# Kernel tuning notes

Measured on AMD Instinct MI355X. Metric: run time of the kernel, lower is better.

Reference implementation:

```python
import jax, jax.numpy as jnp
import numpy as np

EPS = 1e-5
K = 20
MAXV = 64


def knn_idx(x, k):
    # x: [B,N,D] -> idx: [B,N,k] (excluding self, matching torch topk of -dist)
    xx = jnp.sum(x * x, axis=-1, keepdims=True)                      # [B,N,1]
    dist = xx - 2.0 * jnp.einsum('bnd,bmd->bnm', x, x) + jnp.swapaxes(xx, 1, 2)
    _, idx = jax.lax.top_k(-dist, k + 1)
    return idx[:, :, 1:]


def edge_conv(x, W, gamma, beta, mean, var, k):
    # x: [B,N,C]; W: [O,2C]; BN in eval mode; max over k neighbors
    idx = knn_idx(x, k)                                              # [B,N,k]
    nbr = jax.vmap(lambda xi, ii: xi[ii])(x, idx)                    # [B,N,k,C]
    ctr = jnp.broadcast_to(x[:, :, None, :], nbr.shape)
    ef = jnp.concatenate([ctr, nbr - ctr], axis=-1)                  # [B,N,k,2C]
    y = jnp.einsum('bnkc,oc->bnko', ef, W)                           # 1x1 conv
    y = (y - mean) * (gamma * jax.lax.rsqrt(var + EPS)) + beta       # BN eval
    y = jnp.where(y >= 0, y, 0.2 * y)                                # LeakyReLU
    return jnp.max(y, axis=2)                                        # [B,N,O]


def setup_inputs() -> dict:
    key = jax.random.key(0)
    ks = jax.random.split(key, 32)
    f32 = jnp.float32
    def w(k_, o, i):
        return jax.random.normal(k_, (o, i), f32) / np.float32(np.sqrt(i))
    def vec(k_, c):
        return jax.random.normal(k_, (c,), f32) * 0.1
    d = {}
    d['x'] = jax.random.normal(ks[0], (4, 8192, 5), f32)
    # EdgeConv 1: 5 -> 32
    d['W1'] = w(ks[1], 32, 10)
    d['g1'] = jax.random.uniform(ks[2], (32,), f32, 0.5, 1.5)
    d['b1'] = vec(ks[3], 32); d['m1'] = vec(ks[4], 32)
    d['v1'] = jax.random.uniform(ks[5], (32,), f32, 0.5, 1.5)
    # EdgeConv 2: 32 -> 64
    d['W2'] = w(ks[6], 64, 64)
    d['g2'] = jax.random.uniform(ks[7], (64,), f32, 0.5, 1.5)
    d['b2'] = vec(ks[8], 64); d['m2'] = vec(ks[9], 64)
    d['v2'] = jax.random.uniform(ks[10], (64,), f32, 0.5, 1.5)
    # EdgeConv 3: 64 -> 128
    d['W3'] = w(ks[11], 128, 128)
    d['g3'] = jax.random.uniform(ks[12], (128,), f32, 0.5, 1.5)
    d['b3'] = vec(ks[13], 128); d['m3'] = vec(ks[14], 128)
    d['v3'] = jax.random.uniform(ks[15], (128,), f32, 0.5, 1.5)
    # conv_global: 224 -> 256
    d['Wg'] = w(ks[16], 256, 224)
    d['gg'] = jax.random.uniform(ks[17], (256,), f32, 0.5, 1.5)
    d['bg'] = vec(ks[18], 256); d['mg'] = vec(ks[19], 256)
    d['vg'] = jax.random.uniform(ks[20], (256,), f32, 0.5, 1.5)
    # vertex predictor heads
    d['Wv1'] = w(ks[21], 512, 256); d['bv1'] = vec(ks[22], 512)
    d['Wv2'] = w(ks[23], 192, 512); d['bv2'] = vec(ks[24], 192)
    d['Wq1'] = w(ks[25], 64, 256); d['bq1'] = vec(ks[26], 64)
    d['Wq2'] = w(ks[27], 1, 64); d['bq2'] = vec(ks[28], 1)
    return d


def reference(x, W1, g1, b1, m1, v1, W2, g2, b2, m2, v2, W3, g3, b3, m3, v3,
              Wg, gg, bg, mg, vg, Wv1, bv1, Wv2, bv2, Wq1, bq1, Wq2, bq2):
    B = x.shape[0]
    x1 = edge_conv(x, W1, g1, b1, m1, v1, K)      # [B,N,32]
    x2 = edge_conv(x1, W2, g2, b2, m2, v2, K)     # [B,N,64]
    x3 = edge_conv(x2, W3, g3, b3, m3, v3, K)     # [B,N,128]
    x_concat = jnp.concatenate([x1, x2, x3], axis=2)               # [B,N,224]
    xg = jnp.einsum('bnc,oc->bno', x_concat, Wg)                   # 1x1 conv1d
    xg = (xg - mg) * (gg * jax.lax.rsqrt(vg + EPS)) + bg
    xg = jnp.where(xg >= 0, xg, 0.2 * xg)
    gfeat = jnp.max(xg, axis=1)                                    # [B,256]
    h = jax.nn.relu(gfeat @ Wv1.T + bv1)                           # Dropout=eval id
    vertex_coords = (h @ Wv2.T + bv2).reshape(B, MAXV, 3)
    q = jax.nn.relu(gfeat @ Wq1.T + bq1)
    nvs = jax.nn.sigmoid(q @ Wq2.T + bq2)                          # [B,1]
    num_vertices = jnp.clip(jnp.round(nvs * MAXV), 1, MAXV).astype(jnp.int32)
    return (vertex_coords, num_vertices[:, 0], nvs[:, 0], gfeat, x_concat)
```

## Files before the change

### kernel.cpp

```cpp
#include <hip/hip_runtime.h>
#include <hip/hip_bf16.h>


#define NPTS 8192
#define BATCH 4
#define KNBR 20

template <int D, int RS, int S, int TJ, int B>
__global__ __launch_bounds__(128) void knn_part(
    const float* feat, float* xcat) {
    __shared__ float xj[TJ * D];
    __shared__ float xxj[TJ];
    __shared__ float bufd[B * 128];
    __shared__ unsigned short bufj[B * 128];
    const int JC = NPTS / S;

    int gi = blockIdx.x * 128 + threadIdx.x;
    int s  = blockIdx.y;
    int b  = gi >> 13;
    int ib = gi & (NPTS - 1);
    const float* fb = feat + (size_t)b * NPTS * RS;
    int tid = threadIdx.x;

    float xi[D];
    if (D % 4 == 0) {
        #pragma unroll
        for (int c4 = 0; c4 < D / 4; ++c4) {
            float4 v = *(const float4*)(fb + (size_t)ib * RS + 4 * c4);
            xi[4 * c4] = v.x; xi[4 * c4 + 1] = v.y;
            xi[4 * c4 + 2] = v.z; xi[4 * c4 + 3] = v.w;
        }
    } else {
        #pragma unroll
        for (int c = 0; c < D; ++c) xi[c] = fb[(size_t)ib * RS + c];
    }
    float xxi = 0.f;
    #pragma unroll
    for (int c = 0; c < D; ++c) xxi = fmaf(xi[c], xi[c], xxi);

    float dl[21];
    int   il[21];
    #pragma unroll
    for (int t = 0; t < 21; ++t) { dl[t] = __builtin_inff(); il[t] = 0; }

    float thr = __builtin_inff();
    int   cnt = 0;

    for (int j0 = s * JC; j0 < (s + 1) * JC; j0 += TJ) {
        __syncthreads();
        if (D % 4 == 0) {
            for (int e = tid; e < TJ * (D / 4); e += 128) {
                int r = e / (D / 4), c4 = e % (D / 4);
                float4 v = *(const float4*)(fb + (size_t)(j0 + r) * RS + 4 * c4);
                *(float4*)(xj + r * D + 4 * c4) = v;
            }
        } else {
            for (int e = tid; e < TJ * D; e += 128) {
                int r = e / D, c = e % D;
                xj[e] = fb[(size_t)(j0 + r) * RS + c];
            }
        }
        if (tid < TJ) {
            const float* row = fb + (size_t)(j0 + tid) * RS;
            float sm = 0.f;
            if (D % 4 == 0) {
                #pragma unroll
                for (int c4 = 0; c4 < D / 4; ++c4) {
                    float4 v = *(const float4*)(row + 4 * c4);
                    sm = fmaf(v.x, v.x, sm); sm = fmaf(v.y, v.y, sm);
                    sm = fmaf(v.z, v.z, sm); sm = fmaf(v.w, v.w, sm);
                }
            } else {
                #pragma unroll
                for (int c = 0; c < D; ++c) sm = fmaf(row[c], row[c], sm);
            }
            xxj[tid] = sm;
        }
        __syncthreads();
        for (int jj = 0; jj < TJ; ++jj) {
            float dot = 0.f;
            if (D % 4 == 0) {
                const float* xr = xj + jj * D;
                #pragma unroll
                for (int c4 = 0; c4 < D / 4; ++c4) {
                    float4 v = *(const float4*)(xr + 4 * c4);
                    dot = fmaf(xi[4 * c4 + 0], v.x, dot);
                    dot = fmaf(xi[4 * c4 + 1], v.y, dot);
                    dot = fmaf(xi[4 * c4 + 2], v.z, dot);
                    dot = fmaf(xi[4 * c4 + 3], v.w, dot);
                }
            } else {
                #pragma unroll
                for (int c = 0; c < D; ++c) dot = fmaf(xi[c], xj[jj * D + c], dot);
            }
            float d = __builtin_fmaf(-2.f, dot, xxi + xxj[jj]);
            if (__any(cnt == B)) {
                for (int u = 0; u < B; ++u) {
                    if (u < cnt) {
                        float dd = bufd[u * 128 + tid];
                        int   jj2 = (int)bufj[u * 128 + tid];
                        if (dd < dl[20]) {
                            dl[20] = dd; il[20] = jj2;
                            #pragma unroll
                            for (int t = 20; t > 0; --t) {
                                if (dl[t] < dl[t - 1]) {
                                    float td = dl[t]; dl[t] = dl[t - 1]; dl[t - 1] = td;
                                    int   ti = il[t]; il[t] = il[t - 1]; il[t - 1] = ti;
                                }
                            }
                        }
                    }
                }
                cnt = 0;
                thr = dl[20];
            }
            if (d < thr) {
                bufd[cnt * 128 + tid] = d;
                bufj[cnt * 128 + tid] = (unsigned short)(j0 + jj);
                ++cnt;
            }
        }
    }
    for (int u = 0; u < B; ++u) {
        if (u < cnt) {
            float dd = bufd[u * 128 + tid];
            int   jj2 = (int)bufj[u * 128 + tid];
            if (dd < dl[20]) {
                dl[20] = dd; il[20] = jj2;
                #pragma unroll
                for (int t = 20; t > 0; --t) {
                    if (dl[t] < dl[t - 1]) {
                        float td = dl[t]; dl[t] = dl[t - 1]; dl[t - 1] = td;
                        int   ti = il[t]; il[t] = il[t - 1]; il[t - 1] = ti;
                    }
                }
            }
        }
    }
    unsigned short* cp =
        (unsigned short*)(xcat + (size_t)gi * 224 + 96) + s * 21;
    #pragma unroll
    for (int t = 0; t < 21; ++t) cp[t] = (unsigned short)il[t];
}

template <int D, int RS, int S>
__global__ __launch_bounds__(256) void knn_merge(
    const float* feat, const float* xcat, unsigned short* __restrict__ idxout) {
    int gi = blockIdx.x * 256 + threadIdx.x;
    int b  = gi >> 13;
    int ib = gi & (NPTS - 1);
    const float* fb = feat + (size_t)b * NPTS * RS;

    float xi[D];
    if (D % 4 == 0) {
        #pragma unroll
        for (int c4 = 0; c4 < D / 4; ++c4) {
            float4 v = *(const float4*)(fb + (size_t)ib * RS + 4 * c4);
            xi[4 * c4] = v.x; xi[4 * c4 + 1] = v.y;
            xi[4 * c4 + 2] = v.z; xi[4 * c4 + 3] = v.w;
        }
    } else {
        #pragma unroll
        for (int c = 0; c < D; ++c) xi[c] = fb[(size_t)ib * RS + c];
    }
    float xxi = 0.f;
    #pragma unroll
    for (int c = 0; c < D; ++c) xxi = fmaf(xi[c], xi[c], xxi);

    const unsigned short* cp =
        (const unsigned short*)(xcat + (size_t)gi * 224 + 96);

    float dl[21];
    int   il[21];
    #pragma unroll
    for (int t = 0; t < 21; ++t) { dl[t] = __builtin_inff(); il[t] = 0; }

    for (int t = 0; t < S * 21; ++t) {
        int j = ((int)cp[t]) & (NPTS - 1);
        const float* row = fb + (size_t)j * RS;
        float dot = 0.f, xx = 0.f;
        if (D % 4 == 0) {
            #pragma unroll
            for (int c4 = 0; c4 < D / 4; ++c4) {
                float4 v = *(const float4*)(row + 4 * c4);
                dot = fmaf(xi[4 * c4], v.x, dot);     xx = fmaf(v.x, v.x, xx);
                dot = fmaf(xi[4 * c4 + 1], v.y, dot); xx = fmaf(v.y, v.y, xx);
                dot = fmaf(xi[4 * c4 + 2], v.z, dot); xx = fmaf(v.z, v.z, xx);
                dot = fmaf(xi[4 * c4 + 3], v.w, dot); xx = fmaf(v.w, v.w, xx);
            }
        } else {
            #pragma unroll
            for (int c = 0; c < D; ++c) {
                float v = row[c];
                dot = fmaf(xi[c], v, dot);
                xx  = fmaf(v, v, xx);
            }
        }
        float d = __builtin_fmaf(-2.f, dot, xxi + xx);
        if (d < dl[20]) {
            dl[20] = d; il[20] = j;
            #pragma unroll
            for (int u = 20; u > 0; --u) {
                if (dl[u] < dl[u - 1]) {
                    float td = dl[u]; dl[u] = dl[u - 1]; dl[u - 1] = td;
                    int   ti = il[u]; il[u] = il[u - 1]; il[u - 1] = ti;
                }
            }
        }
    }
    unsigned short* op = idxout + (size_t)gi * KNBR;
    #pragma unroll
    for (int t = 1; t < 21; ++t) op[t - 1] = (unsigned short)il[t];
}

template <int CIN, int RS, int COUT, int OTILE, int P>
__global__ __launch_bounds__(256) void edgeconv_kernel(
    const float* feat, const unsigned short* __restrict__ knn,
    const float* __restrict__ W, const float* __restrict__ g,
    const float* __restrict__ beta, const float* __restrict__ mu,
    const float* __restrict__ var,
    float* outb, int concat_off) {
    __shared__ float diff[P][KNBR][CIN];
    __shared__ float xil[P][CIN];
    __shared__ unsigned short kidx[P * KNBR];
    __shared__ float sl[OTILE], bl[OTILE], ml[OTILE];

    int tid = threadIdx.x;
    int h   = blockIdx.y;
    int n0  = blockIdx.x * P;
    int b   = n0 >> 13;
    const float* fbase = feat + ((size_t)b << 13) * RS;

    for (int e = tid; e < P * CIN; e += 256)
        xil[e / CIN][e % CIN] = feat[(size_t)(n0 + e / CIN) * RS + e % CIN];
    for (int e = tid; e < P * KNBR; e += 256)
        kidx[e] = knn[(size_t)(n0 + e / KNBR) * KNBR + e % KNBR] & (NPTS - 1);
    for (int e = tid; e < OTILE; e += 256) {
        int o = h * OTILE + e;
        sl[e] = g[o] * rsqrtf(var[o] + 1e-5f);
        bl[e] = beta[o];
        ml[e] = mu[o];
    }
    __syncthreads();

    if (CIN % 4 == 0) {
        for (int e = tid; e < P * KNBR * (CIN / 4); e += 256) {
            int r = e / (CIN / 4), c4 = e % (CIN / 4);
            int p = r / KNBR, k = r % KNBR;
            int j = (int)kidx[r];
            float4 v = *(const float4*)(fbase + (size_t)j * RS + 4 * c4);
            diff[p][k][4 * c4 + 0] = v.x - xil[p][4 * c4 + 0];
            diff[p][k][4 * c4 + 1] = v.y - xil[p][4 * c4 + 1];
            diff[p][k][4 * c4 + 2] = v.z - xil[p][4 * c4 + 2];
            diff[p][k][4 * c4 + 3] = v.w - xil[p][4 * c4 + 3];
        }
    } else {
        for (int e = tid; e < P * KNBR * CIN; e += 256) {
            int r = e / CIN, c = e % CIN;
            int pp = r / KNBR, k = r % KNBR;
            int j = (int)kidx[r];
            diff[pp][k][c] = fbase[(size_t)j * RS + c] - xil[pp][c];
        }
    }
    __syncthreads();

    int ol = tid % OTILE, p = tid / OTILE;
    int o  = h * OTILE + ol;

    float wreg[CIN];
    #pragma unroll
    for (int c = 0; c < CIN; ++c) wreg[c] = W[(size_t)o * (2 * CIN) + c];
    float a = 0.f;
    #pragma unroll
    for (int c = 0; c < CIN; ++c) a = fmaf(wreg[c], xil[p][c], a);
    #pragma unroll
    for (int c = 0; c < CIN; ++c) wreg[c] = W[(size_t)o * (2 * CIN) + CIN + c];

    float s = sl[ol], mm = ml[ol], bb = bl[ol];
    float best = -__builtin_inff();
    for (int k = 0; k < KNBR; ++k) {
        float ac0 = a, ac1 = 0.f, ac2 = 0.f, ac3 = 0.f;
        #pragma unroll
        for (int c = 0; c < CIN; ++c) {
            float d = diff[p][k][c];
            if ((c & 3) == 0)      ac0 = fmaf(wreg[c], d, ac0);
            else if ((c & 3) == 1) ac1 = fmaf(wreg[c], d, ac1);
            else if ((c & 3) == 2) ac2 = fmaf(wreg[c], d, ac2);
            else                   ac3 = fmaf(wreg[c], d, ac3);
        }
        float acc = ((ac0 + ac1) + ac2) + ac3;
        float y = (acc - mm) * s + bb;
        y = (y >= 0.f) ? y : 0.2f * y;
        best = fmaxf(best, y);
    }
    outb[(size_t)(n0 + p) * 224 + concat_off + o] = best;
}

__global__ __launch_bounds__(256) void convglobal_kernel(
    const float* __restrict__ xcat,
    const float* __restrict__ Wg, const float* __restrict__ gg,
    const float* __restrict__ bg, const float* __restrict__ mg,
    const float* __restrict__ vg,
    float* __restrict__ partial) {
    const int KC = 56, PT = 64, OT = 64, ST = 68;
    __shared__ float flT[KC * ST];
    __shared__ float WlT[KC * ST];
    __shared__ float red[64 * 17];

    int tid = threadIdx.x;
    int oi  = tid & 15, pi = tid >> 4;
    int o0  = blockIdx.y * OT;
    int n0  = blockIdx.x * PT;
    int b   = n0 >> 13;
    int pchunk = blockIdx.x & 127;

    float acc[4][4];
    #pragma unroll
    for (int u = 0; u < 4; ++u)
        #pragma unroll
        for (int v = 0; v < 4; ++v) acc[u][v] = 0.f;

    for (int kc = 0; kc < 224; kc += KC) {
        __syncthreads();
        for (int e = tid; e < PT * (KC / 4); e += 256) {
            int p = e / (KC / 4), c4 = e % (KC / 4);
            float4 v = *(const float4*)(xcat + (size_t)(n0 + p) * 224 + kc + 4 * c4);
            flT[(4 * c4 + 0) * ST + p] = v.x;
            flT[(4 * c4 + 1) * ST + p] = v.y;
            flT[(4 * c4 + 2) * ST + p] = v.z;
            flT[(4 * c4 + 3) * ST + p] = v.w;
        }
        for (int e = tid; e < OT * (KC / 4); e += 256) {
            int o = e / (KC / 4), c4 = e % (KC / 4);
            float4 v = *(const float4*)(Wg + (size_t)(o0 + o) * 224 + kc + 4 * c4);
            WlT[(4 * c4 + 0) * ST + o] = v.x;
            WlT[(4 * c4 + 1) * ST + o] = v.y;
            WlT[(4 * c4 + 2) * ST + o] = v.z;
            WlT[(4 * c4 + 3) * ST + o] = v.w;
        }
        __syncthreads();
        #pragma unroll 8
        for (int c = 0; c < KC; ++c) {
            float4 w4 = *(const float4*)(WlT + c * ST + oi * 4);
            float4 f4 = *(const float4*)(flT + c * ST + pi * 4);
            acc[0][0] = fmaf(w4.x, f4.x, acc[0][0]);
            acc[0][1] = fmaf(w4.x, f4.y, acc[0][1]);
            acc[0][2] = fmaf(w4.x, f4.z, acc[0][2]);
            acc[0][3] = fmaf(w4.x, f4.w, acc[0][3]);
            acc[1][0] = fmaf(w4.y, f4.x, acc[1][0]);
            acc[1][1] = fmaf(w4.y, f4.y, acc[1][1]);
            acc[1][2] = fmaf(w4.y, f4.z, acc[1][2]);
            acc[1][3] = fmaf(w4.y, f4.w, acc[1][3]);
            acc[2][0] = fmaf(w4.z, f4.x, acc[2][0]);
            acc[2][1] = fmaf(w4.z, f4.y, acc[2][1]);
            acc[2][2] = fmaf(w4.z, f4.z, acc[2][2]);
            acc[2][3] = fmaf(w4.z, f4.w, acc[2][3]);
            acc[3][0] = fmaf(w4.w, f4.x, acc[3][0]);
            acc[3][1] = fmaf(w4.w, f4.y, acc[3][1]);
            acc[3][2] = fmaf(w4.w, f4.z, acc[3][2]);
            acc[3][3] = fmaf(w4.w, f4.w, acc[3][3]);
        }
    }
    #pragma unroll
    for (int u = 0; u < 4; ++u) {
        int oL = oi * 4 + u, o = o0 + oL;
        float s = gg[o] * rsqrtf(vg[o] + 1e-5f);
        float mm = mg[o], bb = bg[o];
        float best = -__builtin_inff();
        #pragma unroll
        for (int v = 0; v < 4; ++v) {
            float y = (acc[u][v] - mm) * s + bb;
            y = (y >= 0.f) ? y : 0.2f * y;
            best = fmaxf(best, y);
        }
        red[oL * 17 + pi] = best;
    }
    __syncthreads();
    if (tid < 64) {
        float best = -__builtin_inff();
        #pragma unroll
        for (int q = 0; q < 16; ++q) best = fmaxf(best, red[tid * 17 + q]);
        partial[((size_t)(b * 128 + pchunk)) * 256 + o0 + tid] = best;
    }
}

__global__ void reduce_gfeat_kernel(const float* __restrict__ partial,
                                    float* __restrict__ gfeat,
                                    float* __restrict__ outg) {
    int b = blockIdx.x, o = threadIdx.x;
    float best = -__builtin_inff();
    for (int ch = 0; ch < 128; ++ch)
        best = fmaxf(best, partial[((size_t)b * 128 + ch) * 256 + o]);
    gfeat[b * 256 + o] = best;
    outg[b * 256 + o]  = best;
}

__global__ __launch_bounds__(256) void heads_kernel(
    const float* __restrict__ gfeat,
    const float* __restrict__ Wv1, const float* __restrict__ bv1,
    const float* __restrict__ Wv2, const float* __restrict__ bv2,
    const float* __restrict__ Wq1, const float* __restrict__ bq1,
    const float* __restrict__ Wq2, const float* __restrict__ bq2,
    float* __restrict__ out) {
    int b = blockIdx.x, t = threadIdx.x;
    __shared__ float gf[256], h[512], q[64];
    gf[t] = gfeat[b * 256 + t];
    __syncthreads();
    for (int r = t; r < 512; r += 256) {
        float acc = bv1[r];
        for (int c = 0; c < 256; ++c) acc = fmaf(Wv1[r * 256 + c], gf[c], acc);
        h[r] = fmaxf(acc, 0.f);
    }
    __syncthreads();
    if (t < 192) {
        float acc = bv2[t];
        for (int c = 0; c < 512; ++c) acc = fmaf(Wv2[t * 512 + c], h[c], acc);
        out[b * 192 + t] = acc;
    } else {
        int r = t - 192;
        if (r < 64) {
            float acc = bq1[r];
            for (int c = 0; c < 256; ++c) acc = fmaf(Wq1[r * 256 + c], gf[c], acc);
            q[r] = fmaxf(acc, 0.f);
        }
    }
    __syncthreads();
    if (t == 0) {
        float acc = bq2[0];
        for (int c = 0; c < 64; ++c) acc = fmaf(Wq2[c], q[c], acc);
        float nv = 1.0f / (1.0f + expf(-acc));
        out[772 + b] = nv;
        float num = fminf(fmaxf(rintf(nv * 64.0f), 1.0f), 64.0f);
        out[768 + b] = num;
    }
}

extern "C" void kernel_launch(void* const* d_in, const int* in_sizes, int n_in,
                              void* d_out, int out_size, void* d_ws, size_t ws_size,
                              hipStream_t stream) {
    (void)in_sizes; (void)n_in; (void)out_size; (void)ws_size;
    const float* x   = (const float*)d_in[0];
    const float* W1  = (const float*)d_in[1];
    const float* g1  = (const float*)d_in[2];
    const float* b1  = (const float*)d_in[3];
    const float* m1  = (const float*)d_in[4];
    const float* v1  = (const float*)d_in[5];
    const float* W2  = (const float*)d_in[6];
    const float* g2  = (const float*)d_in[7];
    const float* b2  = (const float*)d_in[8];
    const float* m2  = (const float*)d_in[9];
    const float* v2  = (const float*)d_in[10];
    const float* W3  = (const float*)d_in[11];
    const float* g3  = (const float*)d_in[12];
    const float* b3  = (const float*)d_in[13];
    const float* m3  = (const float*)d_in[14];
    const float* v3  = (const float*)d_in[15];
    const float* Wg  = (const float*)d_in[16];
    const float* gg  = (const float*)d_in[17];
    const float* bg  = (const float*)d_in[18];
    const float* mg  = (const float*)d_in[19];
    const float* vg  = (const float*)d_in[20];
    const float* Wv1 = (const float*)d_in[21];
    const float* bv1 = (const float*)d_in[22];
    const float* Wv2 = (const float*)d_in[23];
    const float* bv2 = (const float*)d_in[24];
    const float* Wq1 = (const float*)d_in[25];
    const float* bq1 = (const float*)d_in[26];
    const float* Wq2 = (const float*)d_in[27];
    const float* bq2 = (const float*)d_in[28];

    float* out  = (float*)d_out;
    float* xcat = out + 1800;
    char* ws = (char*)d_ws;
    const int ROWS = BATCH * NPTS;

    unsigned short* idx  = (unsigned short*)(ws);
    float*          part = (float*)(ws);
    float*          gft  = (float*)(ws + 524288);

    knn_part<5, 5, 8, 128, 8><<<dim3(ROWS / 128, 8), 128, 0, stream>>>(x, xcat);
    knn_merge<5, 5, 8><<<ROWS / 256, 256, 0, stream>>>(x, xcat, idx);
    edgeconv_kernel<5, 5, 32, 32, 8>
        <<<dim3(ROWS / 8, 1), 256, 0, stream>>>(x, idx, W1, g1, b1, m1, v1, xcat, 0);

    knn_part<32, 224, 8, 128, 8><<<dim3(ROWS / 128, 8), 128, 0, stream>>>(xcat, xcat);
    knn_merge<32, 224, 8><<<ROWS / 256, 256, 0, stream>>>(xcat, xcat, idx);
    edgeconv_kernel<32, 224, 64, 64, 4>
        <<<dim3(ROWS / 4, 1), 256, 0, stream>>>(xcat, idx, W2, g2, b2, m2, v2, xcat, 32);

    knn_part<64, 224, 8, 64, 8><<<dim3(ROWS / 128, 8), 128, 0, stream>>>(xcat + 32, xcat);
    knn_merge<64, 224, 8><<<ROWS / 256, 256, 0, stream>>>(xcat + 32, xcat, idx);
    edgeconv_kernel<64, 224, 128, 64, 4>
        <<<dim3(ROWS / 4, 2), 256, 0, stream>>>(xcat + 32, idx, W3, g3, b3, m3, v3, xcat, 96);

    convglobal_kernel<<<dim3(ROWS / 64, 4), 256, 0, stream>>>(
        xcat, Wg, gg, bg, mg, vg, part);
    reduce_gfeat_kernel<<<BATCH, 256, 0, stream>>>(part, gft, out + 776);

    heads_kernel<<<BATCH, 256, 0, stream>>>(
        gft, Wv1, bv1, Wv2, bv2, Wq1, bq1, Wq2, bq2, out);
}
```

Before: 3.783 ms.

## Compute kNN candidate distances with bf16 MFMA and refine exactly in fp32

Replaces the scalar fp32 pairwise-distance loop in the partial kNN kernel with bf16 MFMA 16x16x32 tiles. The resulting distances are stored in swizzled shared memory and filtered against a threshold widened by a safety margin. Surviving candidates are buffered and recomputed exactly in fp32 before insertion into the per-thread top-21 list, so the ranking still comes from full-precision distances. This cuts VALU work for the distance computation, at the cost of larger shared-memory use, lower occupancy, and a margin-based filter that could drop true neighbours if bf16 error exceeds the bound.

```diff
diff --git a/kernel.cpp b/kernel.cpp
--- a/kernel.cpp
+++ b/kernel.cpp
@@ -6,21 +6,54 @@
 #define BATCH 4
 #define KNBR 20
 
-template <int D, int RS, int S, int TJ, int B>
-__global__ __launch_bounds__(128) void knn_part(
+typedef short bf16x8 __attribute__((ext_vector_type(8)));
+typedef float f32x4 __attribute__((ext_vector_type(4)));
+
+__device__ __forceinline__ unsigned short f2bf(float f) {
+    union { float f; unsigned u; } v; v.f = f;
+    unsigned r = v.u + 0x7fffu + ((v.u >> 16) & 1u);
+    return (unsigned short)(r >> 16);
+}
+
+__device__ __forceinline__ int cswz(int r, int nc) {
+    return (nc == 8) ? (r & 7) : ((r >> 1) & 3);
+}
+__device__ __forceinline__ int dswz(int q) { return (q >> 1) & 7; }
+
+template <int D, int DK, int RS, int S>
+__global__ __launch_bounds__(128) void knn_part_mfma(
     const float* feat, float* xcat) {
-    __shared__ float xj[TJ * D];
-    __shared__ float xxj[TJ];
-    __shared__ float bufd[B * 128];
-    __shared__ unsigned short bufj[B * 128];
-    const int JC = NPTS / S;
-
-    int gi = blockIdx.x * 128 + threadIdx.x;
-    int s  = blockIdx.y;
-    int b  = gi >> 13;
-    int ib = gi & (NPTS - 1);
+    constexpr int TJ  = 32;
+    constexpr int BUF = 16;
+    constexpr int JC  = NPTS / S;
+    constexpr int NC  = DK / 8;
+    constexpr int KS  = DK / 32;
+    constexpr int DSTR = 36;
+    constexpr int RSF = (D % 4 == 0) ? D : 9;
+    constexpr int REGA   = 18432;
+    constexpr int OFF_XJF = REGA;
+    constexpr int OFF_XJH = OFF_XJF + ((TJ * RSF * 4 + 15) & ~15);
+    constexpr int OFF_XXJ = OFF_XJH + TJ * DK * 2;
+    constexpr int OFF_BUF = OFF_XXJ + JC * 4;
+    constexpr int OFF_RED = OFF_BUF + BUF * 128 * 2;
+    __shared__ __align__(16) char smem[OFF_RED + 512];
+
+    float*          dist = (float*)smem;
+    unsigned short* xih  = (unsigned short*)smem;
+    float*          xjf  = (float*)(smem + OFF_XJF);
+    unsigned short* xjh  = (unsigned short*)(smem + OFF_XJH);
+    float*          xxj  = (float*)(smem + OFF_XXJ);
+    unsigned short* bufj = (unsigned short*)(smem + OFF_BUF);
+    float*          red  = (float*)(smem + OFF_RED);
+
+    const int tid   = threadIdx.x;
+    const int gi    = blockIdx.x * 128 + tid;
+    const int s     = blockIdx.y;
+    const int b     = gi >> 13;
+    const int ib    = gi & (NPTS - 1);
+    const int n0b   = (blockIdx.x * 128) & (NPTS - 1);
+    const int sbase = s * JC;
     const float* fb = feat + (size_t)b * NPTS * RS;
-    int tid = threadIdx.x;
 
     float xi[D];
     if (D % 4 == 0) {
@@ -38,105 +71,198 @@
     #pragma unroll
     for (int c = 0; c < D; ++c) xxi = fmaf(xi[c], xi[c], xxi);
 
+    for (int e = tid; e < 128 * NC; e += 128) {
+        int r = e / NC, c = e % NC;
+        const float* row = fb + (size_t)(n0b + r) * RS;
+        bf16x8 h;
+        if (D % 8 == 0) {
+            float4 v0 = *(const float4*)(row + c * 8);
+            float4 v1 = *(const float4*)(row + c * 8 + 4);
+            h[0] = (short)f2bf(v0.x); h[1] = (short)f2bf(v0.y);
+            h[2] = (short)f2bf(v0.z); h[3] = (short)f2bf(v0.w);
+            h[4] = (short)f2bf(v1.x); h[5] = (short)f2bf(v1.y);
+            h[6] = (short)f2bf(v1.z); h[7] = (short)f2bf(v1.w);
+        } else {
+            #pragma unroll
+            for (int t = 0; t < 8; ++t) {
+                int dim = c * 8 + t;
+                h[t] = (dim < D) ? (short)f2bf(row[dim]) : (short)0;
+            }
+        }
+        *(bf16x8*)(xih + (size_t)r * DK + (c ^ cswz(r, NC)) * 8) = h;
+    }
+
+    float mymax = 0.f;
+    for (int r = tid; r < JC; r += 128) {
+        const float* row = fb + (size_t)(sbase + r) * RS;
+        float sm = 0.f;
+        if (D % 4 == 0) {
+            #pragma unroll
+            for (int c4 = 0; c4 < D / 4; ++c4) {
+                float4 v = *(const float4*)(row + 4 * c4);
+                sm = fmaf(v.x, v.x, sm); sm = fmaf(v.y, v.y, sm);
+                sm = fmaf(v.z, v.z, sm); sm = fmaf(v.w, v.w, sm);
+            }
+        } else {
+            #pragma unroll
+            for (int c = 0; c < D; ++c) sm = fmaf(row[c], row[c], sm);
+        }
+        xxj[r] = sm;
+        mymax = fmaxf(mymax, sm);
+    }
+    red[tid] = mymax;
+    __syncthreads();
+
+    const int lane = tid & 63, wid = tid >> 6;
+    const int ln = lane & 15, lg = lane >> 4;
+    bf16x8 bfr[4][KS];
+    #pragma unroll
+    for (int qs = 0; qs < 4; ++qs)
+        #pragma unroll
+        for (int ks = 0; ks < KS; ++ks) {
+            int q = wid * 64 + qs * 16 + ln;
+            bfr[qs][ks] = *(const bf16x8*)(
+                xih + (size_t)q * DK + (((lg + 4 * ks) ^ cswz(q, NC)) * 8));
+        }
+
+    #pragma unroll
+    for (int off = 64; off >= 1; off >>= 1) {
+        if (tid < off) red[tid] = fmaxf(red[tid], red[tid + off]);
+        __syncthreads();
+    }
+    const float margin = 0.015625f * (xxi + red[0]);
+
     float dl[21];
     int   il[21];
     #pragma unroll
     for (int t = 0; t < 21; ++t) { dl[t] = __builtin_inff(); il[t] = 0; }
-
-    float thr = __builtin_inff();
+    float thr_s = __builtin_inff();
     int   cnt = 0;
-
-    for (int j0 = s * JC; j0 < (s + 1) * JC; j0 += TJ) {
-        __syncthreads();
-        if (D % 4 == 0) {
-            for (int e = tid; e < TJ * (D / 4); e += 128) {
-                int r = e / (D / 4), c4 = e % (D / 4);
-                float4 v = *(const float4*)(fb + (size_t)(j0 + r) * RS + 4 * c4);
-                *(float4*)(xj + r * D + 4 * c4) = v;
-            }
-        } else {
-            for (int e = tid; e < TJ * D; e += 128) {
-                int r = e / D, c = e % D;
-                xj[e] = fb[(size_t)(j0 + r) * RS + c];
-            }
-        }
-        if (tid < TJ) {
-            const float* row = fb + (size_t)(j0 + tid) * RS;
-            float sm = 0.f;
-            if (D % 4 == 0) {
-                #pragma unroll
-                for (int c4 = 0; c4 < D / 4; ++c4) {
-                    float4 v = *(const float4*)(row + 4 * c4);
-                    sm = fmaf(v.x, v.x, sm); sm = fmaf(v.y, v.y, sm);
-                    sm = fmaf(v.z, v.z, sm); sm = fmaf(v.w, v.w, sm);
+    int   j0s = 0;
+
+    auto drain = [&]() {
+        #pragma unroll 1
+        for (int u = 0; __any(u < cnt); ++u) {
+            if (u < cnt) {
+                int jsp = (int)bufj[u * 128 + tid];
+                int jl  = jsp - j0s;
+                const float* row = xjf + (size_t)jl * RSF;
+                float dot = 0.f;
+                if (D % 4 == 0) {
+                    int fsw = jl & 7;
+                    #pragma unroll
+                    for (int c4 = 0; c4 < D / 4; ++c4) {
+                        float4 v = *(const float4*)(row + ((c4 ^ fsw) * 4));
+                        dot = fmaf(xi[4 * c4 + 0], v.x, dot);
+                        dot = fmaf(xi[4 * c4 + 1], v.y, dot);
+                        dot = fmaf(xi[4 * c4 + 2], v.z, dot);
+                        dot = fmaf(xi[4 * c4 + 3], v.w, dot);
+                    }
+                } else {
+                    #pragma unroll
+                    for (int c = 0; c < D; ++c) dot = fmaf(xi[c], row[c], dot);
                 }
-            } else {
-                #pragma unroll
-                for (int c = 0; c < D; ++c) sm = fmaf(row[c], row[c], sm);
-            }
-            xxj[tid] = sm;
-        }
-        __syncthreads();
-        for (int jj = 0; jj < TJ; ++jj) {
-            float dot = 0.f;
-            if (D % 4 == 0) {
-                const float* xr = xj + jj * D;
-                #pragma unroll
-                for (int c4 = 0; c4 < D / 4; ++c4) {
-                    float4 v = *(const float4*)(xr + 4 * c4);
-                    dot = fmaf(xi[4 * c4 + 0], v.x, dot);
-                    dot = fmaf(xi[4 * c4 + 1], v.y, dot);
-                    dot = fmaf(xi[4 * c4 + 2], v.z, dot);
-                    dot = fmaf(xi[4 * c4 + 3], v.w, dot);
-                }
-            } else {
-                #pragma unroll
-                for (int c = 0; c < D; ++c) dot = fmaf(xi[c], xj[jj * D + c], dot);
-            }
-            float d = __builtin_fmaf(-2.f, dot, xxi + xxj[jj]);
-            if (__any(cnt == B)) {
-                for (int u = 0; u < B; ++u) {
-                    if (u < cnt) {
-                        float dd = bufd[u * 128 + tid];
-                        int   jj2 = (int)bufj[u * 128 + tid];
-                        if (dd < dl[20]) {
-                            dl[20] = dd; il[20] = jj2;
-                            #pragma unroll
-                            for (int t = 20; t > 0; --t) {
-                                if (dl[t] < dl[t - 1]) {
-                                    float td = dl[t]; dl[t] = dl[t - 1]; dl[t - 1] = td;
-                                    int   ti = il[t]; il[t] = il[t - 1]; il[t - 1] = ti;
-                                }
-                            }
+                float dd = __builtin_fmaf(-2.f, dot, xxi + xxj[jsp]);
+                if (dd < dl[20]) {
+                    dl[20] = dd; il[20] = sbase + jsp;
+                    #pragma unroll
+                    for (int t = 20; t > 0; --t) {
+                        if (dl[t] < dl[t - 1]) {
+                            float td = dl[t]; dl[t] = dl[t - 1]; dl[t - 1] = td;
+                            int   ti = il[t]; il[t] = il[t - 1]; il[t - 1] = ti;
                         }
                     }
                 }
-                cnt = 0;
-                thr = dl[20];
-            }
-            if (d < thr) {
-                bufd[cnt * 128 + tid] = d;
-                bufj[cnt * 128 + tid] = (unsigned short)(j0 + jj);
-                ++cnt;
-            }
-        }
-    }
-    for (int u = 0; u < B; ++u) {
-        if (u < cnt) {
-            float dd = bufd[u * 128 + tid];
-            int   jj2 = (int)bufj[u * 128 + tid];
-            if (dd < dl[20]) {
-                dl[20] = dd; il[20] = jj2;
+            }
+        }
+        cnt = 0;
+        thr_s = (dl[20] + margin) - xxi;
+    };
+
+    #pragma unroll 1
+    for (int t0 = 0; t0 < JC; t0 += TJ) {
+        j0s = t0;
+        __syncthreads();
+        if (D % 8 == 0) {
+            for (int e = tid; e < TJ * NC; e += 128) {
+                int r = e / NC, c = e % NC;
+                const float* row = fb + (size_t)(sbase + t0 + r) * RS + c * 8;
+                float4 v0 = *(const float4*)(row);
+                float4 v1 = *(const float4*)(row + 4);
+                int fsw = r & 7;
+                *(float4*)(xjf + (size_t)r * RSF + (((2 * c)     ^ fsw) * 4)) = v0;
+                *(float4*)(xjf + (size_t)r * RSF + (((2 * c + 1) ^ fsw) * 4)) = v1;
+                bf16x8 h;
+                h[0] = (short)f2bf(v0.x); h[1] = (short)f2bf(v0.y);
+                h[2] = (short)f2bf(v0.z); h[3] = (short)f2bf(v0.w);
+                h[4] = (short)f2bf(v1.x); h[5] = (short)f2bf(v1.y);
+                h[6] = (short)f2bf(v1.z); h[7] = (short)f2bf(v1.w);
+                *(bf16x8*)(xjh + (size_t)r * DK + ((c ^ cswz(r, NC)) * 8)) = h;
+            }
+        } else {
+            for (int e = tid; e < TJ * NC; e += 128) {
+                int r = e / NC, c = e % NC;
+                const float* row = fb + (size_t)(sbase + t0 + r) * RS;
+                bf16x8 h;
                 #pragma unroll
-                for (int t = 20; t > 0; --t) {
-                    if (dl[t] < dl[t - 1]) {
-                        float td = dl[t]; dl[t] = dl[t - 1]; dl[t - 1] = td;
-                        int   ti = il[t]; il[t] = il[t - 1]; il[t - 1] = ti;
-                    }
+                for (int q2 = 0; q2 < 8; ++q2) {
+                    int dim = c * 8 + q2;
+                    float f = (dim < D) ? row[dim] : 0.f;
+                    h[q2] = (short)f2bf(f);
+                    if (c == 0 && q2 < D) xjf[(size_t)r * RSF + q2] = f;
                 }
-            }
-        }
-    }
+                *(bf16x8*)(xjh + (size_t)r * DK + ((c ^ cswz(r, NC)) * 8)) = h;
+            }
+        }
+        __syncthreads();
+
+        #pragma unroll
+        for (int js = 0; js < TJ / 16; ++js) {
+            bf16x8 afr[KS];
+            #pragma unroll
+            for (int ks = 0; ks < KS; ++ks) {
+                int jr = js * 16 + ln;
+                afr[ks] = *(const bf16x8*)(
+                    xjh + (size_t)jr * DK +
+                    (((lg + 4 * ks) ^ cswz(jr, NC)) * 8));
+            }
+            float4 xj4 = *(const float4*)(xxj + t0 + js * 16 + lg * 4);
+            #pragma unroll
+            for (int qs = 0; qs < 4; ++qs) {
+                f32x4 acc = {0.f, 0.f, 0.f, 0.f};
+                #pragma unroll
+                for (int ks = 0; ks < KS; ++ks)
+                    acc = __builtin_amdgcn_mfma_f32_16x16x32_bf16(
+                        afr[ks], bfr[qs][ks], acc, 0, 0, 0);
+                float4 sv;
+                sv.x = __builtin_fmaf(-2.f, acc[0], xj4.x);
+                sv.y = __builtin_fmaf(-2.f, acc[1], xj4.y);
+                sv.z = __builtin_fmaf(-2.f, acc[2], xj4.z);
+                sv.w = __builtin_fmaf(-2.f, acc[3], xj4.w);
+                int q  = wid * 64 + qs * 16 + ln;
+                int ck = js * 4 + lg;
+                *(float4*)(dist + (size_t)q * DSTR + ((ck ^ dswz(q)) * 4)) = sv;
+            }
+        }
+        __syncthreads();
+
+        {
+            float* drow = dist + (size_t)tid * DSTR;
+            int dsw = dswz(tid);
+            #pragma unroll 1
+            for (int c = 0; c < TJ / 4; ++c) {
+                if (__any(cnt > BUF - 4)) drain();
+                float4 sv = *(const float4*)(drow + ((c ^ dsw) * 4));
+                int jb = t0 + c * 4;
+                if (sv.x < thr_s) { bufj[cnt * 128 + tid] = (unsigned short)(jb);     ++cnt; }
+                if (sv.y < thr_s) { bufj[cnt * 128 + tid] = (unsigned short)(jb + 1); ++cnt; }
+                if (sv.z < thr_s) { bufj[cnt * 128 + tid] = (unsigned short)(jb + 2); ++cnt; }
+                if (sv.w < thr_s) { bufj[cnt * 128 + tid] = (unsigned short)(jb + 3); ++cnt; }
+            }
+            drain();
+        }
+    }
+
     unsigned short* cp =
         (unsigned short*)(xcat + (size_t)gi * 224 + 96) + s * 21;
     #pragma unroll
@@ -478,17 +604,17 @@
     float*          part = (float*)(ws);
     float*          gft  = (float*)(ws + 524288);
 
-    knn_part<5, 5, 8, 128, 8><<<dim3(ROWS / 128, 8), 128, 0, stream>>>(x, xcat);
+    knn_part_mfma<5, 32, 5, 8><<<dim3(ROWS / 128, 8), 128, 0, stream>>>(x, xcat);
     knn_merge<5, 5, 8><<<ROWS / 256, 256, 0, stream>>>(x, xcat, idx);
     edgeconv_kernel<5, 5, 32, 32, 8>
         <<<dim3(ROWS / 8, 1), 256, 0, stream>>>(x, idx, W1, g1, b1, m1, v1, xcat, 0);
 
-    knn_part<32, 224, 8, 128, 8><<<dim3(ROWS / 128, 8), 128, 0, stream>>>(xcat, xcat);
+    knn_part_mfma<32, 32, 224, 8><<<dim3(ROWS / 128, 8), 128, 0, stream>>>(xcat, xcat);
     knn_merge<32, 224, 8><<<ROWS / 256, 256, 0, stream>>>(xcat, xcat, idx);
     edgeconv_kernel<32, 224, 64, 64, 4>
         <<<dim3(ROWS / 4, 1), 256, 0, stream>>>(xcat, idx, W2, g2, b2, m2, v2, xcat, 32);
 
-    knn_part<64, 224, 8, 64, 8><<<dim3(ROWS / 128, 8), 128, 0, stream>>>(xcat + 32, xcat);
+    knn_part_mfma<64, 64, 224, 8><<<dim3(ROWS / 128, 8), 128, 0, stream>>>(xcat + 32, xcat);
     knn_merge<64, 224, 8><<<ROWS / 256, 256, 0, stream>>>(xcat + 32, xcat, idx);
     edgeconv_kernel<64, 224, 128, 64, 4>
         <<<dim3(ROWS / 4, 2), 256, 0, stream>>>(xcat + 32, idx, W3, g3, b3, m3, v3, xcat, 96);
```

After: 4.896 ms. +29.4%, slower.

## Filter kNN candidates with fast split-accumulator test, recompute exact distance on insert

Applied to the files above, without the earlier changes.

For the 32- and 64-dim kNN passes, the candidate scan now computes distances with four independent accumulators and a relaxed threshold (an EPS margin scaled by the norm sum). It buffers only candidate indices and recomputes the exact sequential-FMA distance from shared memory when inserting into the sorted top-21 list. Shared tiles get an XOR swizzle to reduce bank conflicts, the candidate buffer depth grows from 8 to 16, launch bounds request two blocks per SM, and the drain loops exit early once no lane has pending work. This shortens the FMA dependency chain and removes the distance buffer, at the cost of recomputing dot products for buffered candidates and more register pressure.

```diff
diff --git a/kernel.cpp b/kernel.cpp
--- a/kernel.cpp
+++ b/kernel.cpp
@@ -7,11 +7,12 @@
 #define KNBR 20
 
 template <int D, int RS, int S, int TJ, int B>
-__global__ __launch_bounds__(128) void knn_part(
+__global__ __launch_bounds__(128, 2) void knn_part(
     const float* feat, float* xcat) {
+    constexpr bool PRE = (D % 4 == 0);
     __shared__ float xj[TJ * D];
     __shared__ float xxj[TJ];
-    __shared__ float bufd[B * 128];
+    __shared__ float bufd[PRE ? 1 : B * 128];
     __shared__ unsigned short bufj[B * 128];
     const int JC = NPTS / S;
 
@@ -23,7 +24,7 @@
     int tid = threadIdx.x;
 
     float xi[D];
-    if (D % 4 == 0) {
+    if (PRE) {
         #pragma unroll
         for (int c4 = 0; c4 < D / 4; ++c4) {
             float4 v = *(const float4*)(fb + (size_t)ib * RS + 4 * c4);
@@ -45,88 +46,27 @@
 
     float thr = __builtin_inff();
     int   cnt = 0;
-
-    for (int j0 = s * JC; j0 < (s + 1) * JC; j0 += TJ) {
-        __syncthreads();
-        if (D % 4 == 0) {
-            for (int e = tid; e < TJ * (D / 4); e += 128) {
-                int r = e / (D / 4), c4 = e % (D / 4);
-                float4 v = *(const float4*)(fb + (size_t)(j0 + r) * RS + 4 * c4);
-                *(float4*)(xj + r * D + 4 * c4) = v;
-            }
-        } else {
-            for (int e = tid; e < TJ * D; e += 128) {
-                int r = e / D, c = e % D;
-                xj[e] = fb[(size_t)(j0 + r) * RS + c];
-            }
-        }
-        if (tid < TJ) {
-            const float* row = fb + (size_t)(j0 + tid) * RS;
-            float sm = 0.f;
-            if (D % 4 == 0) {
-                #pragma unroll
-                for (int c4 = 0; c4 < D / 4; ++c4) {
-                    float4 v = *(const float4*)(row + 4 * c4);
-                    sm = fmaf(v.x, v.x, sm); sm = fmaf(v.y, v.y, sm);
-                    sm = fmaf(v.z, v.z, sm); sm = fmaf(v.w, v.w, sm);
-                }
-            } else {
-                #pragma unroll
-                for (int c = 0; c < D; ++c) sm = fmaf(row[c], row[c], sm);
-            }
-            xxj[tid] = sm;
-        }
-        __syncthreads();
-        for (int jj = 0; jj < TJ; ++jj) {
+    int   j0  = 0;
+    const float EPS = 1.52587890625e-05f;
+
+    auto insP = [&](int u) {
+        if (u < cnt) {
+            int j  = (int)bufj[u * 128 + tid];
+            int jl = j - j0;
+            const float* row = xj + (size_t)jl * D;
+            int fsw = jl & 7;
             float dot = 0.f;
-            if (D % 4 == 0) {
-                const float* xr = xj + jj * D;
-                #pragma unroll
-                for (int c4 = 0; c4 < D / 4; ++c4) {
-                    float4 v = *(const float4*)(xr + 4 * c4);
-                    dot = fmaf(xi[4 * c4 + 0], v.x, dot);
-                    dot = fmaf(xi[4 * c4 + 1], v.y, dot);
-                    dot = fmaf(xi[4 * c4 + 2], v.z, dot);
-                    dot = fmaf(xi[4 * c4 + 3], v.w, dot);
-                }
-            } else {
-                #pragma unroll
-                for (int c = 0; c < D; ++c) dot = fmaf(xi[c], xj[jj * D + c], dot);
-            }
-            float d = __builtin_fmaf(-2.f, dot, xxi + xxj[jj]);
-            if (__any(cnt == B)) {
-                for (int u = 0; u < B; ++u) {
-                    if (u < cnt) {
-                        float dd = bufd[u * 128 + tid];
-                        int   jj2 = (int)bufj[u * 128 + tid];
-                        if (dd < dl[20]) {
-                            dl[20] = dd; il[20] = jj2;
-                            #pragma unroll
-                            for (int t = 20; t > 0; --t) {
-                                if (dl[t] < dl[t - 1]) {
-                                    float td = dl[t]; dl[t] = dl[t - 1]; dl[t - 1] = td;
-                                    int   ti = il[t]; il[t] = il[t - 1]; il[t - 1] = ti;
-                                }
-                            }
-                        }
-                    }
-                }
-                cnt = 0;
-                thr = dl[20];
-            }
-            if (d < thr) {
-                bufd[cnt * 128 + tid] = d;
-                bufj[cnt * 128 + tid] = (unsigned short)(j0 + jj);
-                ++cnt;
-            }
-        }
-    }
-    for (int u = 0; u < B; ++u) {
-        if (u < cnt) {
-            float dd = bufd[u * 128 + tid];
-            int   jj2 = (int)bufj[u * 128 + tid];
+            #pragma unroll
+            for (int c4 = 0; c4 < D / 4; ++c4) {
+                float4 v = *(const float4*)(row + ((c4 ^ fsw) * 4));
+                dot = fmaf(xi[4 * c4 + 0], v.x, dot);
+                dot = fmaf(xi[4 * c4 + 1], v.y, dot);
+                dot = fmaf(xi[4 * c4 + 2], v.z, dot);
+                dot = fmaf(xi[4 * c4 + 3], v.w, dot);
+            }
+            float dd = __builtin_fmaf(-2.f, dot, xxi + xxj[jl]);
             if (dd < dl[20]) {
-                dl[20] = dd; il[20] = jj2;
+                dl[20] = dd; il[20] = j;
                 #pragma unroll
                 for (int t = 20; t > 0; --t) {
                     if (dl[t] < dl[t - 1]) {
@@ -136,7 +76,114 @@
                 }
             }
         }
-    }
+    };
+    auto drainP = [&]() {
+        #pragma unroll 1
+        for (int u = 0; __any(u < cnt); u += 2) {
+            insP(u);
+            insP(u + 1);
+        }
+        cnt = 0;
+        thr = dl[20];
+    };
+    auto drainR12 = [&]() {
+        #pragma unroll 1
+        for (int u = 0; __any(u < cnt); ++u) {
+            if (u < cnt) {
+                float dd  = bufd[u * 128 + tid];
+                int   jj2 = (int)bufj[u * 128 + tid];
+                if (dd < dl[20]) {
+                    dl[20] = dd; il[20] = jj2;
+                    #pragma unroll
+                    for (int t = 20; t > 0; --t) {
+                        if (dl[t] < dl[t - 1]) {
+                            float td = dl[t]; dl[t] = dl[t - 1]; dl[t - 1] = td;
+                            int   ti = il[t]; il[t] = il[t - 1]; il[t - 1] = ti;
+                        }
+                    }
+                }
+            }
+        }
+        cnt = 0;
+        thr = dl[20];
+    };
+
+    #pragma unroll 1
+    for (int t0 = s * JC; t0 < (s + 1) * JC; t0 += TJ) {
+        j0 = t0;
+        __syncthreads();
+        if (PRE) {
+            for (int e = tid; e < TJ * (D / 4); e += 128) {
+                int r = e / (D / 4), c4 = e % (D / 4);
+                float4 v = *(const float4*)(fb + (size_t)(t0 + r) * RS + 4 * c4);
+                *(float4*)(xj + (size_t)r * D + (((c4 ^ (r & 7))) * 4)) = v;
+            }
+        } else {
+            for (int e = tid; e < TJ * D; e += 128) {
+                int r = e / D, c = e % D;
+                xj[e] = fb[(size_t)(t0 + r) * RS + c];
+            }
+        }
+        if (tid < TJ) {
+            const float* row = fb + (size_t)(t0 + tid) * RS;
+            float sm = 0.f;
+            if (PRE) {
+                #pragma unroll
+                for (int c4 = 0; c4 < D / 4; ++c4) {
+                    float4 v = *(const float4*)(row + 4 * c4);
+                    sm = fmaf(v.x, v.x, sm); sm = fmaf(v.y, v.y, sm);
+                    sm = fmaf(v.z, v.z, sm); sm = fmaf(v.w, v.w, sm);
+                }
+            } else {
+                #pragma unroll
+                for (int c = 0; c < D; ++c) sm = fmaf(row[c], row[c], sm);
+            }
+            xxj[tid] = sm;
+        }
+        __syncthreads();
+
+        if (PRE) {
+            #pragma unroll 1
+            for (int jj = 0; jj < TJ; ++jj) {
+                float sum = xxi + xxj[jj];
+                const float* xr = xj + (size_t)jj * D;
+                int fsw = jj & 7;
+                float a0 = 0.f, a1 = 0.f, a2 = 0.f, a3 = 0.f;
+                #pragma unroll
+                for (int c4 = 0; c4 < D / 4; ++c4) {
+                    float4 v = *(const float4*)(xr + ((c4 ^ fsw) * 4));
+                    a0 = fmaf(xi[4 * c4 + 0], v.x, a0);
+                    a1 = fmaf(xi[4 * c4 + 1], v.y, a1);
+                    a2 = fmaf(xi[4 * c4 + 2], v.z, a2);
+                    a3 = fmaf(xi[4 * c4 + 3], v.w, a3);
+                }
+                float dot4 = ((a0 + a1) + a2) + a3;
+                float da = __builtin_fmaf(-2.f, dot4, sum);
+                if (__any(cnt == B)) drainP();
+                if (da < __builtin_fmaf(EPS, sum, thr)) {
+                    bufj[cnt * 128 + tid] = (unsigned short)(t0 + jj);
+                    ++cnt;
+                }
+            }
+            drainP();
+        } else {
+            #pragma unroll 1
+            for (int jj = 0; jj < TJ; ++jj) {
+                float dot = 0.f;
+                #pragma unroll
+                for (int c = 0; c < D; ++c) dot = fmaf(xi[c], xj[jj * D + c], dot);
+                float d = __builtin_fmaf(-2.f, dot, xxi + xxj[jj]);
+                if (__any(cnt == B)) drainR12();
+                if (d < thr) {
+                    bufd[cnt * 128 + tid] = d;
+                    bufj[cnt * 128 + tid] = (unsigned short)(t0 + jj);
+                    ++cnt;
+                }
+            }
+        }
+    }
+    if (!PRE) drainR12();
+
     unsigned short* cp =
         (unsigned short*)(xcat + (size_t)gi * 224 + 96) + s * 21;
     #pragma unroll
@@ -483,12 +530,12 @@
     edgeconv_kernel<5, 5, 32, 32, 8>
         <<<dim3(ROWS / 8, 1), 256, 0, stream>>>(x, idx, W1, g1, b1, m1, v1, xcat, 0);
 
-    knn_part<32, 224, 8, 128, 8><<<dim3(ROWS / 128, 8), 128, 0, stream>>>(xcat, xcat);
+    knn_part<32, 224, 8, 128, 16><<<dim3(ROWS / 128, 8), 128, 0, stream>>>(xcat, xcat);
     knn_merge<32, 224, 8><<<ROWS / 256, 256, 0, stream>>>(xcat, xcat, idx);
     edgeconv_kernel<32, 224, 64, 64, 4>
         <<<dim3(ROWS / 4, 1), 256, 0, stream>>>(xcat, idx, W2, g2, b2, m2, v2, xcat, 32);
 
-    knn_part<64, 224, 8, 64, 8><<<dim3(ROWS / 128, 8), 128, 0, stream>>>(xcat + 32, xcat);
+    knn_part<64, 224, 8, 64, 16><<<dim3(ROWS / 128, 8), 128, 0, stream>>>(xcat + 32, xcat);
     knn_merge<64, 224, 8><<<ROWS / 256, 256, 0, stream>>>(xcat + 32, xcat, idx);
     edgeconv_kernel<64, 224, 128, 64, 4>
         <<<dim3(ROWS / 4, 2), 256, 0, stream>>>(xcat + 32, idx, W3, g3, b3, m3, v3, xcat, 96);
```

Measured after the change: 4.309 ms. 13.9% more time.
